# Kernel tuning notes

Hardware: AMD Instinct MI355X
Metric: run time of the kernel (lower is better)

The kernel has to match this reference:

```python
import jax, jax.numpy as jnp
import numpy as np

N_NODES = 100000
N_EDGES = 1600000


def gcn_conv(x, edge_index, W, b):
    """PyG-style GCNConv: self-loops + symmetric normalization + scatter-add."""
    n = x.shape[0]
    src, dst = edge_index[0], edge_index[1]
    loop = jnp.arange(n, dtype=src.dtype)
    src = jnp.concatenate([src, loop])
    dst = jnp.concatenate([dst, loop])
    h = x @ W  # [n, out] transform before propagate (PyG order)
    deg = jax.ops.segment_sum(jnp.ones_like(dst, dtype=h.dtype), dst, num_segments=n)
    dinv = jnp.where(deg > 0, deg ** -0.5, 0.0)
    norm = dinv[src] * dinv[dst]  # [E+n]
    msgs = h[src] * norm[:, None]  # gather + scale (largest intermediate)
    out = jax.ops.segment_sum(msgs, dst, num_segments=n)
    return out + b


def setup_inputs() -> dict:
    key = jax.random.key(0)
    ks = jax.random.split(key, 8)
    edge_attr = jax.random.normal(ks[0], (N_NODES, 5), dtype=jnp.float32)
    edge_index = jax.random.randint(ks[1], (2, N_EDGES), 0, N_NODES, dtype=jnp.int64)
    def lin(k, fan_in, fan_out):
        bound = 1.0 / np.sqrt(fan_in)
        return jax.random.uniform(k, (fan_in, fan_out), jnp.float32, -bound, bound)
    return {
        "edge_attr": edge_attr,
        "edge_index": edge_index,
        "W1": lin(ks[2], 5, 64),
        "b1": jnp.zeros((64,), jnp.float32),
        "W2": lin(ks[3], 64, 32),
        "b2": jnp.zeros((32,), jnp.float32),
        "fcW1": lin(ks[4], 32, 16),
        "fcb1": jnp.zeros((16,), jnp.float32),
        "fcW2": lin(ks[5], 16, 2),
        "fcb2": jnp.zeros((2,), jnp.float32),
    }


def reference(edge_attr, edge_index, W1, b1, W2, b2, fcW1, fcb1, fcW2, fcb2):
    x = jax.nn.relu(gcn_conv(edge_attr, edge_index, W1, b1))
    x = jax.nn.relu(gcn_conv(x, edge_index, W2, b2))
    x = jax.nn.relu(x @ fcW1 + fcb1)
    return x @ fcW2 + fcb2
```

## Files before the change

### kernel.cpp

```cpp
#include <hip/hip_runtime.h>


#define MS_TILE 2048
#define MAXB 512
#define AGG_NODES 32
#define AGG_STAGE 1024

__global__ __launch_bounds__(256) void histA(const int* __restrict__ dst,
                                             int* __restrict__ histG, int E) {
    __shared__ int h[MAXB];
    int t = threadIdx.x;
    h[t] = 0;
    h[t + 256] = 0;
    __syncthreads();
    int base = blockIdx.x * MS_TILE;
    int cnt = min(MS_TILE, E - base);
    for (int k = t; k < cnt; k += 256) atomicAdd(&h[dst[base + k] >> 8], 1);
    __syncthreads();
    histG[blockIdx.x * MAXB + t] = h[t];
    histG[blockIdx.x * MAXB + 256 + t] = h[t + 256];
}

__global__ __launch_bounds__(256) void scanTiles(const int* __restrict__ histG,
                                                 int* __restrict__ offsG,
                                                 int* __restrict__ bucketTotal,
                                                 int nTiles) {
    __shared__ int scn[256];
    int b = blockIdx.x, t = threadIdx.x;
    int run = 0;
    for (int base = 0; base < nTiles; base += 256) {
        int idx = base + t;
        int v = (idx < nTiles) ? histG[idx * MAXB + b] : 0;
        scn[t] = v;
        __syncthreads();
        int incl = v;
        for (int d = 1; d < 256; d <<= 1) {
            int add = (t >= d) ? scn[t - d] : 0;
            __syncthreads();
            incl += add;
            scn[t] = incl;
            __syncthreads();
        }
        if (idx < nTiles) offsG[idx * MAXB + b] = incl - v + run;
        run += scn[255];
        __syncthreads();
    }
    if (t == 0) bucketTotal[b] = run;
}

__global__ __launch_bounds__(256) void multisplit2(
    const int* __restrict__ src, const int* __restrict__ dst,
    const int* __restrict__ histG, const int* __restrict__ offsG,
    const int* __restrict__ btot, int* __restrict__ gbaseOut,
    unsigned* __restrict__ binned, int E) {
    __shared__ unsigned stage[MS_TILE];
    __shared__ unsigned short sb[MS_TILE];
    __shared__ int hoff[MAXB + 1];
    __shared__ int hcur[MAXB];
    __shared__ int gb[MAXB];
    __shared__ int scn[256];
    int t = threadIdx.x;
    int tile = blockIdx.x;
    int base = tile * MS_TILE;
    int cnt = min(MS_TILE, E - base);

    int b0 = btot[2 * t], b1v = btot[2 * t + 1];
    int s2 = b0 + b1v;
    scn[t] = s2;
    __syncthreads();
    int incl2 = s2;
    for (int d = 1; d < 256; d <<= 1) {
        int add = (t >= d) ? scn[t - d] : 0;
        __syncthreads();
        incl2 += add;
        scn[t] = incl2;
        __syncthreads();
    }
    int ex2 = incl2 - s2;
    gb[2 * t] = ex2 + offsG[tile * MAXB + 2 * t];
    gb[2 * t + 1] = ex2 + b0 + offsG[tile * MAXB + 2 * t + 1];
    if (tile == 0) {
        gbaseOut[2 * t] = ex2;
        gbaseOut[2 * t + 1] = ex2 + b0;
        if (t == 255) gbaseOut[MAXB] = E;
    }

    int a0 = histG[tile * MAXB + 2 * t];
    int a1 = histG[tile * MAXB + 2 * t + 1];
    int s = a0 + a1;
    scn[t] = s;
    __syncthreads();
    int incl = s;
    for (int d = 1; d < 256; d <<= 1) {
        int add = (t >= d) ? scn[t - d] : 0;
        __syncthreads();
        incl += add;
        scn[t] = incl;
        __syncthreads();
    }
    int ex = incl - s;
    hoff[2 * t] = ex;
    hoff[2 * t + 1] = ex + a0;
    hcur[2 * t] = ex;
    hcur[2 * t + 1] = ex + a0;
    if (t == 255) hoff[MAXB] = cnt;
    __syncthreads();
    for (int k = t; k < cnt; k += 256) {
        int d = dst[base + k];
        int b = d >> 8;
        int p = atomicAdd(&hcur[b], 1);
        stage[p] = ((unsigned)src[base + k] << 8) | (unsigned)(d & 255);
        sb[p] = (unsigned short)b;
    }
    __syncthreads();
    for (int k = t; k < cnt; k += 256) {
        int b = sb[k];
        binned[gb[b] + (k - hoff[b])] = stage[k];
    }
}

__global__ __launch_bounds__(256) void place_fine2(
    const unsigned* __restrict__ binned, const int* __restrict__ gbase,
    const float* __restrict__ x, int* __restrict__ offs,
    float* __restrict__ dinv, float* __restrict__ y, int* __restrict__ srcs, int n) {
    __shared__ int cnt[256];
    __shared__ int scn[256];
    __shared__ int lcur[256];
    int t = threadIdx.x, b = blockIdx.x;
    int node0 = b << 8;
    int nn = min(256, n - node0);
    int e0 = gbase[b], e1 = gbase[b + 1];
    cnt[t] = 0;
    __syncthreads();
    for (int k = e0 + t; k < e1; k += 256) atomicAdd(&cnt[binned[k] & 255u], 1);
    __syncthreads();
    int c = cnt[t];
    scn[t] = c;
    __syncthreads();
    int incl = c;
    for (int d = 1; d < 256; d <<= 1) {
        int add = (t >= d) ? scn[t - d] : 0;
        __syncthreads();
        incl += add;
        scn[t] = incl;
        __syncthreads();
    }
    int myoff = e0 + (incl - c);
    lcur[t] = myoff;
    if (t < nn) {
        int node = node0 + t;
        offs[node] = myoff;
        float di = 1.0f / sqrtf((float)(c + 1));
        dinv[node] = di;
        const float* xr = x + (size_t)node * 5;
        float4 a = {xr[0] * di, xr[1] * di, xr[2] * di, xr[3] * di};
        float4 bq = {xr[4] * di, 0.f, 0.f, 0.f};
        *(float4*)(y + (size_t)node * 8) = a;
        *(float4*)(y + (size_t)node * 8 + 4) = bq;
    }
    __syncthreads();
    for (int k = e0 + t; k < e1; k += 256) {
        unsigned w = binned[k];
        int p = atomicAdd(&lcur[w & 255u], 1);
        srcs[p] = (int)(w >> 8);
    }
}

__global__ __launch_bounds__(128) void agg_xin(
    const float* __restrict__ y, const int* __restrict__ srcs,
    const int* __restrict__ offs, const float* __restrict__ dinv,
    float* __restrict__ z, int n, int E) {
    int i = blockIdx.x * 128 + threadIdx.x;
    if (i >= n) return;
    const float4* yv = (const float4*)y;
    float4 a = yv[(size_t)i * 2];
    float4 b = yv[(size_t)i * 2 + 1];
    int off = offs[i];
    int cnt = ((i + 1 < n) ? offs[i + 1] : E) - off;
    int p = 0;
    for (; p + 4 <= cnt; p += 4) {
        int s0 = srcs[off + p], s1 = srcs[off + p + 1];
        int s2 = srcs[off + p + 2], s3 = srcs[off + p + 3];
        float4 v0 = yv[(size_t)s0 * 2];
        float4 w0 = yv[(size_t)s0 * 2 + 1];
        float4 v1 = yv[(size_t)s1 * 2];
        float4 w1 = yv[(size_t)s1 * 2 + 1];
        float4 v2 = yv[(size_t)s2 * 2];
        float4 w2 = yv[(size_t)s2 * 2 + 1];
        float4 v3 = yv[(size_t)s3 * 2];
        float4 w3 = yv[(size_t)s3 * 2 + 1];
        a.x += (v0.x + v1.x) + (v2.x + v3.x);
        a.y += (v0.y + v1.y) + (v2.y + v3.y);
        a.z += (v0.z + v1.z) + (v2.z + v3.z);
        a.w += (v0.w + v1.w) + (v2.w + v3.w);
        b.x += (w0.x + w1.x) + (w2.x + w3.x);
    }
    for (; p < cnt; ++p) {
        int s0 = srcs[off + p];
        float4 v0 = yv[(size_t)s0 * 2];
        float w0 = y[(size_t)s0 * 8 + 4];
        a.x += v0.x; a.y += v0.y; a.z += v0.z; a.w += v0.w;
        b.x += w0;
    }
    float di = dinv[i];
    float4 oa = {a.x * di, a.y * di, a.z * di, a.w * di};
    float4 ob = {b.x * di, 0.f, 0.f, 0.f};
    float4* zv = (float4*)z;
    zv[(size_t)i * 2] = oa;
    zv[(size_t)i * 2 + 1] = ob;
}

__global__ __launch_bounds__(256) void transform12(
    const float* __restrict__ z, const float* __restrict__ W1,
    const float* __restrict__ b1, const float* __restrict__ W2,
    const float* __restrict__ dinv, float* __restrict__ h2, int n) {
    __shared__ float w1s[320];
    __shared__ float b1s[64];
    __shared__ float w2s[64 * 32];
    __shared__ float o1[32 * 64];
    int t = threadIdx.x;
    w1s[t] = W1[t];
    if (t < 64) {
        w1s[t + 256] = W1[t + 256];
        b1s[t] = b1[t];
    }
#pragma unroll
    for (int r = 0; r < 8; ++r) w2s[r * 256 + t] = W2[r * 256 + t];
    __syncthreads();
    int node0 = blockIdx.x * 32;
#pragma unroll
    for (int r = 0; r < 8; ++r) {
        int idx = r * 256 + t;
        int li = idx >> 6, f = idx & 63;
        int i = node0 + li;
        if (i < n) {
            const float* zr = z + (size_t)i * 8;
            float acc = b1s[f];
#pragma unroll
            for (int k = 0; k < 5; ++k) acc += zr[k] * w1s[k * 64 + f];
            o1[li * 64 + f] = fmaxf(acc, 0.0f);
        }
    }
    __syncthreads();
#pragma unroll
    for (int r = 0; r < 4; ++r) {
        int idx = r * 256 + t;
        int li = idx >> 5, g = idx & 31;
        int i = node0 + li;
        if (i < n) {
            float acc = 0.f;
#pragma unroll
            for (int k = 0; k < 64; ++k) acc += o1[li * 64 + k] * w2s[k * 32 + g];
            h2[(size_t)i * 32 + g] = acc * dinv[i];
        }
    }
}

__global__ __launch_bounds__(256) void agg2_fc(
    const float* __restrict__ h, const int* __restrict__ srcs,
    const int* __restrict__ offs, const float* __restrict__ dinv,
    const float* __restrict__ b2, const float* __restrict__ fcW1,
    const float* __restrict__ fcb1, const float* __restrict__ fcW2,
    const float* __restrict__ fcb2, float* __restrict__ out, int n, int E) {
    __shared__ int sidx[AGG_STAGE];
    __shared__ float sm[AGG_NODES * 33];
    __shared__ float x3s[AGG_NODES * 16];
    __shared__ float w1s[512];
    __shared__ float w2s[32];
    __shared__ float b1s[16];
    __shared__ float b2s[2];
    __shared__ float bs2[32];
    int t = threadIdx.x;
    w1s[t] = fcW1[t];
    w1s[t + 256] = fcW1[t + 256];
    if (t < 32) { w2s[t] = fcW2[t]; bs2[t] = b2[t]; }
    if (t < 16) b1s[t] = fcb1[t];
    if (t < 2) b2s[t] = fcb2[t];

    int node0 = blockIdx.x * AGG_NODES;
    int li = t >> 3, fq = t & 7;
    int i = node0 + li;
    bool live = (i < n);
    const char* hb = (const char*)h;

    int e0 = offs[node0];
    int eEnd = (node0 + AGG_NODES < n) ? offs[node0 + AGG_NODES] : E;
    int myOff = 0, myCnt = 0;
    float4 acc = {0.f, 0.f, 0.f, 0.f};
    if (live) {
        myOff = offs[i];
        myCnt = ((i + 1 < n) ? offs[i + 1] : E) - myOff;
        acc = *(const float4*)(hb + ((size_t)i << 7) + (fq << 4));
    }

    for (int cs = e0; cs < eEnd; cs += AGG_STAGE) {
        int ce = min(cs + AGG_STAGE, eEnd);
        for (int k = cs + t; k < ce; k += 256) sidx[k - cs] = srcs[k] << 7;
        __syncthreads();
        int ps = max(myOff, cs), pe = min(myOff + myCnt, ce);
        int p = ps;
        for (; p + 8 <= pe; p += 8) {
            int o[8];
#pragma unroll
            for (int u = 0; u < 8; ++u) o[u] = sidx[p + u - cs];
            float4 v[8];
#pragma unroll
            for (int u = 0; u < 8; ++u)
                v[u] = *(const float4*)(hb + o[u] + (fq << 4));
#pragma unroll
            for (int u = 0; u < 8; ++u) {
                acc.x += v[u].x; acc.y += v[u].y;
                acc.z += v[u].z; acc.w += v[u].w;
            }
        }
        for (; p + 4 <= pe; p += 4) {
            int o0 = sidx[p - cs], o1 = sidx[p + 1 - cs];
            int o2 = sidx[p + 2 - cs], o3 = sidx[p + 3 - cs];
            float4 v0 = *(const float4*)(hb + o0 + (fq << 4));
            float4 v1 = *(const float4*)(hb + o1 + (fq << 4));
            float4 v2 = *(const float4*)(hb + o2 + (fq << 4));
            float4 v3 = *(const float4*)(hb + o3 + (fq << 4));
            acc.x += (v0.x + v1.x) + (v2.x + v3.x);
            acc.y += (v0.y + v1.y) + (v2.y + v3.y);
            acc.z += (v0.z + v1.z) + (v2.z + v3.z);
            acc.w += (v0.w + v1.w) + (v2.w + v3.w);
        }
        for (; p < pe; ++p) {
            float4 v = *(const float4*)(hb + sidx[p - cs] + (fq << 4));
            acc.x += v.x; acc.y += v.y; acc.z += v.z; acc.w += v.w;
        }
        __syncthreads();
    }

    if (live) {
        float di = dinv[i];
        int f0 = fq << 2;
        sm[li * 33 + f0 + 0] = fmaxf(di * acc.x + bs2[f0 + 0], 0.f);
        sm[li * 33 + f0 + 1] = fmaxf(di * acc.y + bs2[f0 + 1], 0.f);
        sm[li * 33 + f0 + 2] = fmaxf(di * acc.z + bs2[f0 + 2], 0.f);
        sm[li * 33 + f0 + 3] = fmaxf(di * acc.w + bs2[f0 + 3], 0.f);
    }
    __syncthreads();
#pragma unroll
    for (int r = 0; r < 2; ++r) {
        int idx = r * 256 + t;
        int lj = idx >> 4, j = idx & 15;
        if (node0 + lj < n) {
            float a = b1s[j];
#pragma unroll
            for (int k = 0; k < 32; ++k) a += sm[lj * 33 + k] * w1s[k * 16 + j];
            x3s[lj * 16 + j] = fmaxf(a, 0.f);
        }
    }
    __syncthreads();
    if (t < 64) {
        int lj = t >> 1, o = t & 1;
        if (node0 + lj < n) {
            float a = b2s[o];
#pragma unroll
            for (int j = 0; j < 16; ++j) a += x3s[lj * 16 + j] * w2s[j * 2 + o];
            out[(size_t)(node0 + lj) * 2 + o] = a;
        }
    }
}

extern "C" void kernel_launch(void* const* d_in, const int* in_sizes, int n_in,
                              void* d_out, int out_size, void* d_ws, size_t ws_size,
                              hipStream_t stream) {
    const float* edge_attr = (const float*)d_in[0];
    const int* edge_index  = (const int*)d_in[1];
    const float* W1   = (const float*)d_in[2];
    const float* b1   = (const float*)d_in[3];
    const float* W2   = (const float*)d_in[4];
    const float* b2   = (const float*)d_in[5];
    const float* fcW1 = (const float*)d_in[6];
    const float* fcb1 = (const float*)d_in[7];
    const float* fcW2 = (const float*)d_in[8];
    const float* fcb2 = (const float*)d_in[9];
    float* out = (float*)d_out;

    int n = in_sizes[0] / 5;
    int E = in_sizes[1] / 2;
    int NBkt = (n + 255) >> 8;
    int nTiles = (E + MS_TILE - 1) / MS_TILE;
    const int* src = edge_index;
    const int* dst = edge_index + E;

    char* ws = (char*)d_ws;
    auto alloc = [&](size_t bytes) {
        char* p = ws;
        ws += (bytes + 255) & ~(size_t)255;
        return p;
    };
    int*      offs   = (int*)alloc((size_t)n * 4);
    float*    dinv   = (float*)alloc((size_t)n * 4);
    int*      histG  = (int*)alloc((size_t)nTiles * MAXB * 4);
    int*      offsG  = (int*)alloc((size_t)nTiles * MAXB * 4);
    int*      btot   = (int*)alloc((size_t)MAXB * 4);
    int*      gbase  = (int*)alloc((size_t)(MAXB + 1) * 4);
    int*      srcs   = (int*)alloc((size_t)E * 4);
    unsigned* binned = (unsigned*)alloc((size_t)E * 4);
    float*    y      = (float*)alloc((size_t)n * 8 * 4);
    float*    z      = (float*)alloc((size_t)n * 8 * 4);
    float*    h2     = (float*)alloc((size_t)n * 32 * 4);

    histA<<<nTiles, 256, 0, stream>>>(dst, histG, E);
    scanTiles<<<MAXB, 256, 0, stream>>>(histG, offsG, btot, nTiles);
    multisplit2<<<nTiles, 256, 0, stream>>>(src, dst, histG, offsG, btot, gbase,
                                            binned, E);
    place_fine2<<<NBkt, 256, 0, stream>>>(binned, gbase, edge_attr, offs, dinv,
                                          y, srcs, n);
    agg_xin<<<(n + 127) / 128, 128, 0, stream>>>(y, srcs, offs, dinv, z, n, E);
    transform12<<<(n + 31) / 32, 256, 0, stream>>>(z, W1, b1, W2, dinv, h2, n);
    agg2_fc<<<(n + AGG_NODES - 1) / AGG_NODES, 256, 0, stream>>>(
        h2, srcs, offs, dinv, b2, fcW1, fcb1, fcW2, fcb2, out, n, E);
}
```

Baseline: 198.3 us.

## Split each node's edges across two thread groups in layer-2 aggregation; widen first gather

The fused layer-2 aggregation kernel now handles 16 nodes per block, giving each node 16 threads. Two 8-thread groups take alternate edges and combine their partial sums with a wave shuffle, which adds parallelism and memory-level parallelism for each node's gather. The layer-1 gather loop is unrolled from 4 to 8 edges and now loads only the five needed floats per neighbour instead of two full float4s. The risk is twice as many blocks, plus extra offset loads and the staging of srcs indices repeated across more blocks.

Measured after the change: 201.3 us. About the same (+1.5%).

```diff
diff --git a/kernel.cpp b/kernel.cpp
--- a/kernel.cpp
+++ b/kernel.cpp
@@ -3,7 +3,7 @@
 
 #define MS_TILE 2048
 #define MAXB 512
-#define AGG_NODES 32
+#define AGG_NODES 16
 #define AGG_STAGE 1024
 
 __global__ __launch_bounds__(256) void histA(const int* __restrict__ dst,
@@ -178,22 +178,22 @@
     int off = offs[i];
     int cnt = ((i + 1 < n) ? offs[i + 1] : E) - off;
     int p = 0;
-    for (; p + 4 <= cnt; p += 4) {
-        int s0 = srcs[off + p], s1 = srcs[off + p + 1];
-        int s2 = srcs[off + p + 2], s3 = srcs[off + p + 3];
-        float4 v0 = yv[(size_t)s0 * 2];
-        float4 w0 = yv[(size_t)s0 * 2 + 1];
-        float4 v1 = yv[(size_t)s1 * 2];
-        float4 w1 = yv[(size_t)s1 * 2 + 1];
-        float4 v2 = yv[(size_t)s2 * 2];
-        float4 w2 = yv[(size_t)s2 * 2 + 1];
-        float4 v3 = yv[(size_t)s3 * 2];
-        float4 w3 = yv[(size_t)s3 * 2 + 1];
-        a.x += (v0.x + v1.x) + (v2.x + v3.x);
-        a.y += (v0.y + v1.y) + (v2.y + v3.y);
-        a.z += (v0.z + v1.z) + (v2.z + v3.z);
-        a.w += (v0.w + v1.w) + (v2.w + v3.w);
-        b.x += (w0.x + w1.x) + (w2.x + w3.x);
+    for (; p + 8 <= cnt; p += 8) {
+        int s[8];
+#pragma unroll
+        for (int u = 0; u < 8; ++u) s[u] = srcs[off + p + u];
+        float4 v[8];
+        float w[8];
+#pragma unroll
+        for (int u = 0; u < 8; ++u) {
+            v[u] = yv[(size_t)s[u] * 2];
+            w[u] = y[(size_t)s[u] * 8 + 4];
+        }
+#pragma unroll
+        for (int u = 0; u < 8; ++u) {
+            a.x += v[u].x; a.y += v[u].y; a.z += v[u].z; a.w += v[u].w;
+            b.x += w[u];
+        }
     }
     for (; p < cnt; ++p) {
         int s0 = srcs[off + p];
@@ -278,7 +278,9 @@
     if (t < 2) b2s[t] = fcb2[t];
 
     int node0 = blockIdx.x * AGG_NODES;
-    int li = t >> 3, fq = t & 7;
+    int li = t >> 4;
+    int sub = (t >> 3) & 1;
+    int fq = t & 7;
     int i = node0 + li;
     bool live = (i < n);
     const char* hb = (const char*)h;
@@ -290,7 +292,8 @@
     if (live) {
         myOff = offs[i];
         myCnt = ((i + 1 < n) ? offs[i + 1] : E) - myOff;
-        acc = *(const float4*)(hb + ((size_t)i << 7) + (fq << 4));
+        if (sub == 0)
+            acc = *(const float4*)(hb + ((size_t)i << 7) + (fq << 4));
     }
 
     for (int cs = e0; cs < eEnd; cs += AGG_STAGE) {
@@ -298,24 +301,12 @@
         for (int k = cs + t; k < ce; k += 256) sidx[k - cs] = srcs[k] << 7;
         __syncthreads();
         int ps = max(myOff, cs), pe = min(myOff + myCnt, ce);
-        int p = ps;
-        for (; p + 8 <= pe; p += 8) {
-            int o[8];
-#pragma unroll
-            for (int u = 0; u < 8; ++u) o[u] = sidx[p + u - cs];
-            float4 v[8];
-#pragma unroll
-            for (int u = 0; u < 8; ++u)
-                v[u] = *(const float4*)(hb + o[u] + (fq << 4));
-#pragma unroll
-            for (int u = 0; u < 8; ++u) {
-                acc.x += v[u].x; acc.y += v[u].y;
-                acc.z += v[u].z; acc.w += v[u].w;
-            }
-        }
-        for (; p + 4 <= pe; p += 4) {
-            int o0 = sidx[p - cs], o1 = sidx[p + 1 - cs];
-            int o2 = sidx[p + 2 - cs], o3 = sidx[p + 3 - cs];
+        int p = ps + sub;
+        for (; p + 6 < pe; p += 8) {
+            int o0 = sidx[p - cs];
+            int o1 = sidx[p + 2 - cs];
+            int o2 = sidx[p + 4 - cs];
+            int o3 = sidx[p + 6 - cs];
             float4 v0 = *(const float4*)(hb + o0 + (fq << 4));
             float4 v1 = *(const float4*)(hb + o1 + (fq << 4));
             float4 v2 = *(const float4*)(hb + o2 + (fq << 4));
@@ -325,14 +316,19 @@
             acc.z += (v0.z + v1.z) + (v2.z + v3.z);
             acc.w += (v0.w + v1.w) + (v2.w + v3.w);
         }
-        for (; p < pe; ++p) {
+        for (; p < pe; p += 2) {
             float4 v = *(const float4*)(hb + sidx[p - cs] + (fq << 4));
             acc.x += v.x; acc.y += v.y; acc.z += v.z; acc.w += v.w;
         }
         __syncthreads();
     }
 
-    if (live) {
+    int lane = t & 63;
+    acc.x += __shfl(acc.x, lane ^ 8, 64);
+    acc.y += __shfl(acc.y, lane ^ 8, 64);
+    acc.z += __shfl(acc.z, lane ^ 8, 64);
+    acc.w += __shfl(acc.w, lane ^ 8, 64);
+    if (live && sub == 0) {
         float di = dinv[i];
         int f0 = fq << 2;
         sm[li * 33 + f0 + 0] = fmaxf(di * acc.x + bs2[f0 + 0], 0.f);
@@ -341,10 +337,8 @@
         sm[li * 33 + f0 + 3] = fmaxf(di * acc.w + bs2[f0 + 3], 0.f);
     }
     __syncthreads();
-#pragma unroll
-    for (int r = 0; r < 2; ++r) {
-        int idx = r * 256 + t;
-        int lj = idx >> 4, j = idx & 15;
+    {
+        int lj = t >> 4, j = t & 15;
         if (node0 + lj < n) {
             float a = b1s[j];
 #pragma unroll
@@ -353,7 +347,7 @@
         }
     }
     __syncthreads();
-    if (t < 64) {
+    if (t < 32) {
         int lj = t >> 1, o = t & 1;
         if (node0 + lj < n) {
             float a = b2s[o];
```

## Fuse all GCN stages into one cooperative persistent kernel with grid syncs

Applied to the files above, without the earlier changes.

Replaces the seven separate kernel launches with a single cooperative kernel that runs every stage as a grid-stride loop, with grid.sync() between stages. The aim is to remove per-launch overhead and the gaps between kernels. In exchange, the grid is capped at 768 persistent blocks, each block's shared memory is sized for the largest stage, and register pressure from the merged code may lower occupancy and parallelism in the bandwidth-bound gather stages.

Measured after the change: 604.2 us. +204.7%, slower.

```diff
diff --git a/kernel.cpp b/kernel.cpp
--- a/kernel.cpp
+++ b/kernel.cpp
@@ -1,365 +1,383 @@
 #include <hip/hip_runtime.h>
+#include <hip/hip_cooperative_groups.h>
+
+namespace cg = cooperative_groups;
 
 
 #define MS_TILE 2048
 #define MAXB 512
-#define AGG_NODES 32
 #define AGG_STAGE 1024
-
-__global__ __launch_bounds__(256) void histA(const int* __restrict__ dst,
-                                             int* __restrict__ histG, int E) {
-    __shared__ int h[MAXB];
+#define SMEM_BYTES 19712
+
+struct GcnParams {
+    const float* x;
+    const int* src;
+    const int* dst;
+    const float* W1; const float* b1;
+    const float* W2; const float* b2;
+    const float* fcW1; const float* fcb1;
+    const float* fcW2; const float* fcb2;
+    float* out;
+    int* histG; int* offsG; int* btot; int* gbase;
+    unsigned* binned; int* offs; float* dinv;
+    float* y; float* z; float* h2; int* srcs;
+    int n, E, nTiles, NBkt;
+};
+
+__global__ __launch_bounds__(256) void gcn_mono(GcnParams p) {
+    cg::grid_group grid = cg::this_grid();
+    __shared__ __align__(16) unsigned char smem[SMEM_BYTES];
     int t = threadIdx.x;
-    h[t] = 0;
-    h[t + 256] = 0;
-    __syncthreads();
-    int base = blockIdx.x * MS_TILE;
-    int cnt = min(MS_TILE, E - base);
-    for (int k = t; k < cnt; k += 256) atomicAdd(&h[dst[base + k] >> 8], 1);
-    __syncthreads();
-    histG[blockIdx.x * MAXB + t] = h[t];
-    histG[blockIdx.x * MAXB + 256 + t] = h[t + 256];
-}
-
-__global__ __launch_bounds__(256) void scanTiles(const int* __restrict__ histG,
-                                                 int* __restrict__ offsG,
-                                                 int* __restrict__ bucketTotal,
-                                                 int nTiles) {
-    __shared__ int scn[256];
-    int b = blockIdx.x, t = threadIdx.x;
-    int run = 0;
-    for (int base = 0; base < nTiles; base += 256) {
-        int idx = base + t;
-        int v = (idx < nTiles) ? histG[idx * MAXB + b] : 0;
-        scn[t] = v;
+    int G = gridDim.x;
+
+    {
+        int* h = (int*)smem;
+        for (int tile = blockIdx.x; tile < p.nTiles; tile += G) {
+            h[t] = 0;
+            h[t + 256] = 0;
+            __syncthreads();
+            int base = tile * MS_TILE;
+            int cnt = min(MS_TILE, p.E - base);
+            for (int k = t; k < cnt; k += 256) atomicAdd(&h[p.dst[base + k] >> 8], 1);
+            __syncthreads();
+            p.histG[tile * MAXB + t] = h[t];
+            p.histG[tile * MAXB + 256 + t] = h[t + 256];
+        }
+    }
+    grid.sync();
+
+    {
+        int* scn = (int*)smem;
+        for (int b = blockIdx.x; b < MAXB; b += G) {
+            int run = 0;
+            for (int base = 0; base < p.nTiles; base += 256) {
+                int idx = base + t;
+                int v = (idx < p.nTiles) ? p.histG[idx * MAXB + b] : 0;
+                scn[t] = v;
+                __syncthreads();
+                int incl = v;
+                for (int d = 1; d < 256; d <<= 1) {
+                    int add = (t >= d) ? scn[t - d] : 0;
+                    __syncthreads();
+                    incl += add;
+                    scn[t] = incl;
+                    __syncthreads();
+                }
+                if (idx < p.nTiles) p.offsG[idx * MAXB + b] = incl - v + run;
+                run += scn[255];
+                __syncthreads();
+            }
+            if (t == 0) p.btot[b] = run;
+        }
+    }
+    grid.sync();
+
+    {
+        unsigned* stage = (unsigned*)smem;
+        unsigned short* sb = (unsigned short*)(smem + 8192);
+        int* hoff = (int*)(smem + 12288);
+        int* hcur = (int*)(smem + 14344);
+        int* gb   = (int*)(smem + 16392);
+        int* scn  = (int*)(smem + 18440);
+        int b0 = p.btot[2 * t], b1v = p.btot[2 * t + 1];
+        int s2 = b0 + b1v;
+        scn[t] = s2;
         __syncthreads();
-        int incl = v;
+        int incl2 = s2;
         for (int d = 1; d < 256; d <<= 1) {
             int add = (t >= d) ? scn[t - d] : 0;
             __syncthreads();
-            incl += add;
-            scn[t] = incl;
-            __syncthreads();
-        }
-        if (idx < nTiles) offsG[idx * MAXB + b] = incl - v + run;
-        run += scn[255];
+            incl2 += add;
+            scn[t] = incl2;
+            __syncthreads();
+        }
+        int ex2a = incl2 - s2;
+        int ex2b = ex2a + b0;
+        if (blockIdx.x == 0) {
+            p.gbase[2 * t] = ex2a;
+            p.gbase[2 * t + 1] = ex2b;
+            if (t == 255) p.gbase[MAXB] = p.E;
+        }
+        for (int tile = blockIdx.x; tile < p.nTiles; tile += G) {
+            int base = tile * MS_TILE;
+            int cnt = min(MS_TILE, p.E - base);
+            int a0 = p.histG[tile * MAXB + 2 * t];
+            int a1 = p.histG[tile * MAXB + 2 * t + 1];
+            int s = a0 + a1;
+            scn[t] = s;
+            __syncthreads();
+            int incl = s;
+            for (int d = 1; d < 256; d <<= 1) {
+                int add = (t >= d) ? scn[t - d] : 0;
+                __syncthreads();
+                incl += add;
+                scn[t] = incl;
+                __syncthreads();
+            }
+            int ex = incl - s;
+            hoff[2 * t] = ex;
+            hoff[2 * t + 1] = ex + a0;
+            hcur[2 * t] = ex;
+            hcur[2 * t + 1] = ex + a0;
+            gb[2 * t] = ex2a + p.offsG[tile * MAXB + 2 * t];
+            gb[2 * t + 1] = ex2b + p.offsG[tile * MAXB + 2 * t + 1];
+            if (t == 255) hoff[MAXB] = cnt;
+            __syncthreads();
+            for (int k = t; k < cnt; k += 256) {
+                int d = p.dst[base + k];
+                int b = d >> 8;
+                int q = atomicAdd(&hcur[b], 1);
+                stage[q] = ((unsigned)p.src[base + k] << 8) | (unsigned)(d & 255);
+                sb[q] = (unsigned short)b;
+            }
+            __syncthreads();
+            for (int k = t; k < cnt; k += 256) {
+                int b = sb[k];
+                p.binned[gb[b] + (k - hoff[b])] = stage[k];
+            }
+        }
+    }
+    grid.sync();
+
+    {
+        int* cnt  = (int*)smem;
+        int* scn  = (int*)(smem + 1024);
+        int* lcur = (int*)(smem + 2048);
+        for (int b = blockIdx.x; b < p.NBkt; b += G) {
+            int node0 = b << 8;
+            int nn = min(256, p.n - node0);
+            int e0 = p.gbase[b], e1 = p.gbase[b + 1];
+            cnt[t] = 0;
+            __syncthreads();
+            for (int k = e0 + t; k < e1; k += 256)
+                atomicAdd(&cnt[p.binned[k] & 255u], 1);
+            __syncthreads();
+            int c = cnt[t];
+            scn[t] = c;
+            __syncthreads();
+            int incl = c;
+            for (int d = 1; d < 256; d <<= 1) {
+                int add = (t >= d) ? scn[t - d] : 0;
+                __syncthreads();
+                incl += add;
+                scn[t] = incl;
+                __syncthreads();
+            }
+            int myoff = e0 + (incl - c);
+            lcur[t] = myoff;
+            if (t < nn) {
+                int node = node0 + t;
+                p.offs[node] = myoff;
+                float di = 1.0f / sqrtf((float)(c + 1));
+                p.dinv[node] = di;
+                const float* xr = p.x + (size_t)node * 5;
+                float4 va = {xr[0] * di, xr[1] * di, xr[2] * di, xr[3] * di};
+                float4 vb = {xr[4] * di, 0.f, 0.f, 0.f};
+                *(float4*)(p.y + (size_t)node * 8) = va;
+                *(float4*)(p.y + (size_t)node * 8 + 4) = vb;
+            }
+            __syncthreads();
+            for (int k = e0 + t; k < e1; k += 256) {
+                unsigned w = p.binned[k];
+                int q = atomicAdd(&lcur[w & 255u], 1);
+                p.srcs[q] = (int)(w >> 8);
+            }
+            __syncthreads();
+        }
+    }
+    grid.sync();
+
+    {
+        const float4* yv = (const float4*)p.y;
+        for (int i = blockIdx.x * 256 + t; i < p.n; i += G * 256) {
+            float4 a = yv[(size_t)i * 2];
+            float4 b = yv[(size_t)i * 2 + 1];
+            int off = p.offs[i];
+            int cnt = ((i + 1 < p.n) ? p.offs[i + 1] : p.E) - off;
+            int q = 0;
+            for (; q + 4 <= cnt; q += 4) {
+                int s0 = p.srcs[off + q], s1 = p.srcs[off + q + 1];
+                int s2 = p.srcs[off + q + 2], s3 = p.srcs[off + q + 3];
+                float4 v0 = yv[(size_t)s0 * 2];
+                float4 w0 = yv[(size_t)s0 * 2 + 1];
+                float4 v1 = yv[(size_t)s1 * 2];
+                float4 w1 = yv[(size_t)s1 * 2 + 1];
+                float4 v2 = yv[(size_t)s2 * 2];
+                float4 w2 = yv[(size_t)s2 * 2 + 1];
+                float4 v3 = yv[(size_t)s3 * 2];
+                float4 w3 = yv[(size_t)s3 * 2 + 1];
+                a.x += (v0.x + v1.x) + (v2.x + v3.x);
+                a.y += (v0.y + v1.y) + (v2.y + v3.y);
+                a.z += (v0.z + v1.z) + (v2.z + v3.z);
+                a.w += (v0.w + v1.w) + (v2.w + v3.w);
+                b.x += (w0.x + w1.x) + (w2.x + w3.x);
+            }
+            for (; q < cnt; ++q) {
+                int s0 = p.srcs[off + q];
+                float4 v0 = yv[(size_t)s0 * 2];
+                float w0 = p.y[(size_t)s0 * 8 + 4];
+                a.x += v0.x; a.y += v0.y; a.z += v0.z; a.w += v0.w;
+                b.x += w0;
+            }
+            float di = p.dinv[i];
+            float4 oa = {a.x * di, a.y * di, a.z * di, a.w * di};
+            float4 ob = {b.x * di, 0.f, 0.f, 0.f};
+            ((float4*)p.z)[(size_t)i * 2] = oa;
+            ((float4*)p.z)[(size_t)i * 2 + 1] = ob;
+        }
+    }
+    grid.sync();
+
+    {
+        float* w1s = (float*)smem;
+        float* b1s = (float*)(smem + 1280);
+        float* w2s = (float*)(smem + 1536);
+        float* o1  = (float*)(smem + 9728);
+        w1s[t] = p.W1[t];
+        if (t < 64) {
+            w1s[t + 256] = p.W1[t + 256];
+            b1s[t] = p.b1[t];
+        }
+#pragma unroll
+        for (int r = 0; r < 8; ++r) w2s[r * 256 + t] = p.W2[r * 256 + t];
         __syncthreads();
-    }
-    if (t == 0) bucketTotal[b] = run;
-}
-
-__global__ __launch_bounds__(256) void multisplit2(
-    const int* __restrict__ src, const int* __restrict__ dst,
-    const int* __restrict__ histG, const int* __restrict__ offsG,
-    const int* __restrict__ btot, int* __restrict__ gbaseOut,
-    unsigned* __restrict__ binned, int E) {
-    __shared__ unsigned stage[MS_TILE];
-    __shared__ unsigned short sb[MS_TILE];
-    __shared__ int hoff[MAXB + 1];
-    __shared__ int hcur[MAXB];
-    __shared__ int gb[MAXB];
-    __shared__ int scn[256];
-    int t = threadIdx.x;
-    int tile = blockIdx.x;
-    int base = tile * MS_TILE;
-    int cnt = min(MS_TILE, E - base);
-
-    int b0 = btot[2 * t], b1v = btot[2 * t + 1];
-    int s2 = b0 + b1v;
-    scn[t] = s2;
-    __syncthreads();
-    int incl2 = s2;
-    for (int d = 1; d < 256; d <<= 1) {
-        int add = (t >= d) ? scn[t - d] : 0;
+        int nChunks = (p.n + 31) / 32;
+        for (int c = blockIdx.x; c < nChunks; c += G) {
+            int node0 = c * 32;
+#pragma unroll
+            for (int r = 0; r < 8; ++r) {
+                int idx = r * 256 + t;
+                int li = idx >> 6, f = idx & 63;
+                int i = node0 + li;
+                if (i < p.n) {
+                    const float* zr = p.z + (size_t)i * 8;
+                    float acc = b1s[f];
+#pragma unroll
+                    for (int k = 0; k < 5; ++k) acc += zr[k] * w1s[k * 64 + f];
+                    o1[li * 64 + f] = fmaxf(acc, 0.0f);
+                }
+            }
+            __syncthreads();
+#pragma unroll
+            for (int r = 0; r < 4; ++r) {
+                int idx = r * 256 + t;
+                int li = idx >> 5, g = idx & 31;
+                int i = node0 + li;
+                if (i < p.n) {
+                    float acc = 0.f;
+#pragma unroll
+                    for (int k = 0; k < 64; ++k)
+                        acc += o1[li * 64 + k] * w2s[k * 32 + g];
+                    p.h2[(size_t)i * 32 + g] = acc * p.dinv[i];
+                }
+            }
+            __syncthreads();
+        }
+    }
+    grid.sync();
+
+    {
+        int* sidx  = (int*)smem;
+        float* sm  = (float*)(smem + 4096);
+        float* x3s = (float*)(smem + 8320);
+        float* w1s = (float*)(smem + 10368);
+        float* w2s = (float*)(smem + 12416);
+        float* b1s = (float*)(smem + 12544);
+        float* b2s = (float*)(smem + 12608);
+        float* bs2 = (float*)(smem + 12624);
+        w1s[t] = p.fcW1[t];
+        w1s[t + 256] = p.fcW1[t + 256];
+        if (t < 32) { w2s[t] = p.fcW2[t]; bs2[t] = p.b2[t]; }
+        if (t < 16) b1s[t] = p.fcb1[t];
+        if (t < 2) b2s[t] = p.fcb2[t];
         __syncthreads();
-        incl2 += add;
-        scn[t] = incl2;
-        __syncthreads();
-    }
-    int ex2 = incl2 - s2;
-    gb[2 * t] = ex2 + offsG[tile * MAXB + 2 * t];
-    gb[2 * t + 1] = ex2 + b0 + offsG[tile * MAXB + 2 * t + 1];
-    if (tile == 0) {
-        gbaseOut[2 * t] = ex2;
-        gbaseOut[2 * t + 1] = ex2 + b0;
-        if (t == 255) gbaseOut[MAXB] = E;
-    }
-
-    int a0 = histG[tile * MAXB + 2 * t];
-    int a1 = histG[tile * MAXB + 2 * t + 1];
-    int s = a0 + a1;
-    scn[t] = s;
-    __syncthreads();
-    int incl = s;
-    for (int d = 1; d < 256; d <<= 1) {
-        int add = (t >= d) ? scn[t - d] : 0;
-        __syncthreads();
-        incl += add;
-        scn[t] = incl;
-        __syncthreads();
-    }
-    int ex = incl - s;
-    hoff[2 * t] = ex;
-    hoff[2 * t + 1] = ex + a0;
-    hcur[2 * t] = ex;
-    hcur[2 * t + 1] = ex + a0;
-    if (t == 255) hoff[MAXB] = cnt;
-    __syncthreads();
-    for (int k = t; k < cnt; k += 256) {
-        int d = dst[base + k];
-        int b = d >> 8;
-        int p = atomicAdd(&hcur[b], 1);
-        stage[p] = ((unsigned)src[base + k] << 8) | (unsigned)(d & 255);
-        sb[p] = (unsigned short)b;
-    }
-    __syncthreads();
-    for (int k = t; k < cnt; k += 256) {
-        int b = sb[k];
-        binned[gb[b] + (k - hoff[b])] = stage[k];
-    }
-}
-
-__global__ __launch_bounds__(256) void place_fine2(
-    const unsigned* __restrict__ binned, const int* __restrict__ gbase,
-    const float* __restrict__ x, int* __restrict__ offs,
-    float* __restrict__ dinv, float* __restrict__ y, int* __restrict__ srcs, int n) {
-    __shared__ int cnt[256];
-    __shared__ int scn[256];
-    __shared__ int lcur[256];
-    int t = threadIdx.x, b = blockIdx.x;
-    int node0 = b << 8;
-    int nn = min(256, n - node0);
-    int e0 = gbase[b], e1 = gbase[b + 1];
-    cnt[t] = 0;
-    __syncthreads();
-    for (int k = e0 + t; k < e1; k += 256) atomicAdd(&cnt[binned[k] & 255u], 1);
-    __syncthreads();
-    int c = cnt[t];
-    scn[t] = c;
-    __syncthreads();
-    int incl = c;
-    for (int d = 1; d < 256; d <<= 1) {
-        int add = (t >= d) ? scn[t - d] : 0;
-        __syncthreads();
-        incl += add;
-        scn[t] = incl;
-        __syncthreads();
-    }
-    int myoff = e0 + (incl - c);
-    lcur[t] = myoff;
-    if (t < nn) {
-        int node = node0 + t;
-        offs[node] = myoff;
-        float di = 1.0f / sqrtf((float)(c + 1));
-        dinv[node] = di;
-        const float* xr = x + (size_t)node * 5;
-        float4 a = {xr[0] * di, xr[1] * di, xr[2] * di, xr[3] * di};
-        float4 bq = {xr[4] * di, 0.f, 0.f, 0.f};
-        *(float4*)(y + (size_t)node * 8) = a;
-        *(float4*)(y + (size_t)node * 8 + 4) = bq;
-    }
-    __syncthreads();
-    for (int k = e0 + t; k < e1; k += 256) {
-        unsigned w = binned[k];
-        int p = atomicAdd(&lcur[w & 255u], 1);
-        srcs[p] = (int)(w >> 8);
-    }
-}
-
-__global__ __launch_bounds__(128) void agg_xin(
-    const float* __restrict__ y, const int* __restrict__ srcs,
-    const int* __restrict__ offs, const float* __restrict__ dinv,
-    float* __restrict__ z, int n, int E) {
-    int i = blockIdx.x * 128 + threadIdx.x;
-    if (i >= n) return;
-    const float4* yv = (const float4*)y;
-    float4 a = yv[(size_t)i * 2];
-    float4 b = yv[(size_t)i * 2 + 1];
-    int off = offs[i];
-    int cnt = ((i + 1 < n) ? offs[i + 1] : E) - off;
-    int p = 0;
-    for (; p + 4 <= cnt; p += 4) {
-        int s0 = srcs[off + p], s1 = srcs[off + p + 1];
-        int s2 = srcs[off + p + 2], s3 = srcs[off + p + 3];
-        float4 v0 = yv[(size_t)s0 * 2];
-        float4 w0 = yv[(size_t)s0 * 2 + 1];
-        float4 v1 = yv[(size_t)s1 * 2];
-        float4 w1 = yv[(size_t)s1 * 2 + 1];
-        float4 v2 = yv[(size_t)s2 * 2];
-        float4 w2 = yv[(size_t)s2 * 2 + 1];
-        float4 v3 = yv[(size_t)s3 * 2];
-        float4 w3 = yv[(size_t)s3 * 2 + 1];
-        a.x += (v0.x + v1.x) + (v2.x + v3.x);
-        a.y += (v0.y + v1.y) + (v2.y + v3.y);
-        a.z += (v0.z + v1.z) + (v2.z + v3.z);
-        a.w += (v0.w + v1.w) + (v2.w + v3.w);
-        b.x += (w0.x + w1.x) + (w2.x + w3.x);
-    }
-    for (; p < cnt; ++p) {
-        int s0 = srcs[off + p];
-        float4 v0 = yv[(size_t)s0 * 2];
-        float w0 = y[(size_t)s0 * 8 + 4];
-        a.x += v0.x; a.y += v0.y; a.z += v0.z; a.w += v0.w;
-        b.x += w0;
-    }
-    float di = dinv[i];
-    float4 oa = {a.x * di, a.y * di, a.z * di, a.w * di};
-    float4 ob = {b.x * di, 0.f, 0.f, 0.f};
-    float4* zv = (float4*)z;
-    zv[(size_t)i * 2] = oa;
-    zv[(size_t)i * 2 + 1] = ob;
-}
-
-__global__ __launch_bounds__(256) void transform12(
-    const float* __restrict__ z, const float* __restrict__ W1,
-    const float* __restrict__ b1, const float* __restrict__ W2,
-    const float* __restrict__ dinv, float* __restrict__ h2, int n) {
-    __shared__ float w1s[320];
-    __shared__ float b1s[64];
-    __shared__ float w2s[64 * 32];
-    __shared__ float o1[32 * 64];
-    int t = threadIdx.x;
-    w1s[t] = W1[t];
-    if (t < 64) {
-        w1s[t + 256] = W1[t + 256];
-        b1s[t] = b1[t];
-    }
-#pragma unroll
-    for (int r = 0; r < 8; ++r) w2s[r * 256 + t] = W2[r * 256 + t];
-    __syncthreads();
-    int node0 = blockIdx.x * 32;
-#pragma unroll
-    for (int r = 0; r < 8; ++r) {
-        int idx = r * 256 + t;
-        int li = idx >> 6, f = idx & 63;
-        int i = node0 + li;
-        if (i < n) {
-            const float* zr = z + (size_t)i * 8;
-            float acc = b1s[f];
-#pragma unroll
-            for (int k = 0; k < 5; ++k) acc += zr[k] * w1s[k * 64 + f];
-            o1[li * 64 + f] = fmaxf(acc, 0.0f);
-        }
-    }
-    __syncthreads();
-#pragma unroll
-    for (int r = 0; r < 4; ++r) {
-        int idx = r * 256 + t;
-        int li = idx >> 5, g = idx & 31;
-        int i = node0 + li;
-        if (i < n) {
-            float acc = 0.f;
-#pragma unroll
-            for (int k = 0; k < 64; ++k) acc += o1[li * 64 + k] * w2s[k * 32 + g];
-            h2[(size_t)i * 32 + g] = acc * dinv[i];
-        }
-    }
-}
-
-__global__ __launch_bounds__(256) void agg2_fc(
-    const float* __restrict__ h, const int* __restrict__ srcs,
-    const int* __restrict__ offs, const float* __restrict__ dinv,
-    const float* __restrict__ b2, const float* __restrict__ fcW1,
-    const float* __restrict__ fcb1, const float* __restrict__ fcW2,
-    const float* __restrict__ fcb2, float* __restrict__ out, int n, int E) {
-    __shared__ int sidx[AGG_STAGE];
-    __shared__ float sm[AGG_NODES * 33];
-    __shared__ float x3s[AGG_NODES * 16];
-    __shared__ float w1s[512];
-    __shared__ float w2s[32];
-    __shared__ float b1s[16];
-    __shared__ float b2s[2];
-    __shared__ float bs2[32];
-    int t = threadIdx.x;
-    w1s[t] = fcW1[t];
-    w1s[t + 256] = fcW1[t + 256];
-    if (t < 32) { w2s[t] = fcW2[t]; bs2[t] = b2[t]; }
-    if (t < 16) b1s[t] = fcb1[t];
-    if (t < 2) b2s[t] = fcb2[t];
-
-    int node0 = blockIdx.x * AGG_NODES;
-    int li = t >> 3, fq = t & 7;
-    int i = node0 + li;
-    bool live = (i < n);
-    const char* hb = (const char*)h;
-
-    int e0 = offs[node0];
-    int eEnd = (node0 + AGG_NODES < n) ? offs[node0 + AGG_NODES] : E;
-    int myOff = 0, myCnt = 0;
-    float4 acc = {0.f, 0.f, 0.f, 0.f};
-    if (live) {
-        myOff = offs[i];
-        myCnt = ((i + 1 < n) ? offs[i + 1] : E) - myOff;
-        acc = *(const float4*)(hb + ((size_t)i << 7) + (fq << 4));
-    }
-
-    for (int cs = e0; cs < eEnd; cs += AGG_STAGE) {
-        int ce = min(cs + AGG_STAGE, eEnd);
-        for (int k = cs + t; k < ce; k += 256) sidx[k - cs] = srcs[k] << 7;
-        __syncthreads();
-        int ps = max(myOff, cs), pe = min(myOff + myCnt, ce);
-        int p = ps;
-        for (; p + 8 <= pe; p += 8) {
-            int o[8];
-#pragma unroll
-            for (int u = 0; u < 8; ++u) o[u] = sidx[p + u - cs];
-            float4 v[8];
-#pragma unroll
-            for (int u = 0; u < 8; ++u)
-                v[u] = *(const float4*)(hb + o[u] + (fq << 4));
-#pragma unroll
-            for (int u = 0; u < 8; ++u) {
-                acc.x += v[u].x; acc.y += v[u].y;
-                acc.z += v[u].z; acc.w += v[u].w;
-            }
-        }
-        for (; p + 4 <= pe; p += 4) {
-            int o0 = sidx[p - cs], o1 = sidx[p + 1 - cs];
-            int o2 = sidx[p + 2 - cs], o3 = sidx[p + 3 - cs];
-            float4 v0 = *(const float4*)(hb + o0 + (fq << 4));
-            float4 v1 = *(const float4*)(hb + o1 + (fq << 4));
-            float4 v2 = *(const float4*)(hb + o2 + (fq << 4));
-            float4 v3 = *(const float4*)(hb + o3 + (fq << 4));
-            acc.x += (v0.x + v1.x) + (v2.x + v3.x);
-            acc.y += (v0.y + v1.y) + (v2.y + v3.y);
-            acc.z += (v0.z + v1.z) + (v2.z + v3.z);
-            acc.w += (v0.w + v1.w) + (v2.w + v3.w);
-        }
-        for (; p < pe; ++p) {
-            float4 v = *(const float4*)(hb + sidx[p - cs] + (fq << 4));
-            acc.x += v.x; acc.y += v.y; acc.z += v.z; acc.w += v.w;
-        }
-        __syncthreads();
-    }
-
-    if (live) {
-        float di = dinv[i];
-        int f0 = fq << 2;
-        sm[li * 33 + f0 + 0] = fmaxf(di * acc.x + bs2[f0 + 0], 0.f);
-        sm[li * 33 + f0 + 1] = fmaxf(di * acc.y + bs2[f0 + 1], 0.f);
-        sm[li * 33 + f0 + 2] = fmaxf(di * acc.z + bs2[f0 + 2], 0.f);
-        sm[li * 33 + f0 + 3] = fmaxf(di * acc.w + bs2[f0 + 3], 0.f);
-    }
-    __syncthreads();
-#pragma unroll
-    for (int r = 0; r < 2; ++r) {
-        int idx = r * 256 + t;
-        int lj = idx >> 4, j = idx & 15;
-        if (node0 + lj < n) {
-            float a = b1s[j];
-#pragma unroll
-            for (int k = 0; k < 32; ++k) a += sm[lj * 33 + k] * w1s[k * 16 + j];
-            x3s[lj * 16 + j] = fmaxf(a, 0.f);
-        }
-    }
-    __syncthreads();
-    if (t < 64) {
-        int lj = t >> 1, o = t & 1;
-        if (node0 + lj < n) {
-            float a = b2s[o];
-#pragma unroll
-            for (int j = 0; j < 16; ++j) a += x3s[lj * 16 + j] * w2s[j * 2 + o];
-            out[(size_t)(node0 + lj) * 2 + o] = a;
+        const char* hb = (const char*)p.h2;
+        int li = t >> 3, fq = t & 7;
+        int nBlk = (p.n + 31) / 32;
+        for (int bb = blockIdx.x; bb < nBlk; bb += G) {
+            int node0 = bb * 32;
+            int i = node0 + li;
+            bool live = (i < p.n);
+            int e0 = p.offs[node0];
+            int eEnd = (node0 + 32 < p.n) ? p.offs[node0 + 32] : p.E;
+            int myOff = 0, myCnt = 0;
+            float4 acc = {0.f, 0.f, 0.f, 0.f};
+            if (live) {
+                myOff = p.offs[i];
+                myCnt = ((i + 1 < p.n) ? p.offs[i + 1] : p.E) - myOff;
+                acc = *(const float4*)(hb + ((size_t)i << 7) + (fq << 4));
+            }
+            for (int cs = e0; cs < eEnd; cs += AGG_STAGE) {
+                int ce = min(cs + AGG_STAGE, eEnd);
+                for (int k = cs + t; k < ce; k += 256) sidx[k - cs] = p.srcs[k] << 7;
+                __syncthreads();
+                int ps = max(myOff, cs), pe = min(myOff + myCnt, ce);
+                int q = ps;
+                for (; q + 8 <= pe; q += 8) {
+                    int o[8];
+#pragma unroll
+                    for (int u = 0; u < 8; ++u) o[u] = sidx[q + u - cs];
+                    float4 v[8];
+#pragma unroll
+                    for (int u = 0; u < 8; ++u)
+                        v[u] = *(const float4*)(hb + o[u] + (fq << 4));
+#pragma unroll
+                    for (int u = 0; u < 8; ++u) {
+                        acc.x += v[u].x; acc.y += v[u].y;
+                        acc.z += v[u].z; acc.w += v[u].w;
+                    }
+                }
+                for (; q + 4 <= pe; q += 4) {
+                    int o0 = sidx[q - cs], o1 = sidx[q + 1 - cs];
+                    int o2 = sidx[q + 2 - cs], o3 = sidx[q + 3 - cs];
+                    float4 v0 = *(const float4*)(hb + o0 + (fq << 4));
+                    float4 v1 = *(const float4*)(hb + o1 + (fq << 4));
+                    float4 v2 = *(const float4*)(hb + o2 + (fq << 4));
+                    float4 v3 = *(const float4*)(hb + o3 + (fq << 4));
+                    acc.x += (v0.x + v1.x) + (v2.x + v3.x);
+                    acc.y += (v0.y + v1.y) + (v2.y + v3.y);
+                    acc.z += (v0.z + v1.z) + (v2.z + v3.z);
+                    acc.w += (v0.w + v1.w) + (v2.w + v3.w);
+                }
+                for (; q < pe; ++q) {
+                    float4 v = *(const float4*)(hb + sidx[q - cs] + (fq << 4));
+                    acc.x += v.x; acc.y += v.y; acc.z += v.z; acc.w += v.w;
+                }
+                __syncthreads();
+            }
+            if (live) {
+                float di = p.dinv[i];
+                int f0 = fq << 2;
+                sm[li * 33 + f0 + 0] = fmaxf(di * acc.x + bs2[f0 + 0], 0.f);
+                sm[li * 33 + f0 + 1] = fmaxf(di * acc.y + bs2[f0 + 1], 0.f);
+                sm[li * 33 + f0 + 2] = fmaxf(di * acc.z + bs2[f0 + 2], 0.f);
+                sm[li * 33 + f0 + 3] = fmaxf(di * acc.w + bs2[f0 + 3], 0.f);
+            }
+            __syncthreads();
+#pragma unroll
+            for (int r = 0; r < 2; ++r) {
+                int idx = r * 256 + t;
+                int lj = idx >> 4, j = idx & 15;
+                if (node0 + lj < p.n) {
+                    float a = b1s[j];
+#pragma unroll
+                    for (int k = 0; k < 32; ++k)
+                        a += sm[lj * 33 + k] * w1s[k * 16 + j];
+                    x3s[lj * 16 + j] = fmaxf(a, 0.f);
+                }
+            }
+            __syncthreads();
+            if (t < 64) {
+                int lj = t >> 1, o = t & 1;
+                if (node0 + lj < p.n) {
+                    float a = b2s[o];
+#pragma unroll
+                    for (int j = 0; j < 16; ++j)
+                        a += x3s[lj * 16 + j] * w2s[j * 2 + o];
+                    p.out[(size_t)(node0 + lj) * 2 + o] = a;
+                }
+            }
+            __syncthreads();
         }
     }
 }
@@ -367,51 +385,52 @@
 extern "C" void kernel_launch(void* const* d_in, const int* in_sizes, int n_in,
                               void* d_out, int out_size, void* d_ws, size_t ws_size,
                               hipStream_t stream) {
-    const float* edge_attr = (const float*)d_in[0];
-    const int* edge_index  = (const int*)d_in[1];
-    const float* W1   = (const float*)d_in[2];
-    const float* b1   = (const float*)d_in[3];
-    const float* W2   = (const float*)d_in[4];
-    const float* b2   = (const float*)d_in[5];
-    const float* fcW1 = (const float*)d_in[6];
-    const float* fcb1 = (const float*)d_in[7];
-    const float* fcW2 = (const float*)d_in[8];
-    const float* fcb2 = (const float*)d_in[9];
-    float* out = (float*)d_out;
-
-    int n = in_sizes[0] / 5;
-    int E = in_sizes[1] / 2;
-    int NBkt = (n + 255) >> 8;
-    int nTiles = (E + MS_TILE - 1) / MS_TILE;
-    const int* src = edge_index;
-    const int* dst = edge_index + E;
+    GcnParams p;
+    p.x    = (const float*)d_in[0];
+    const int* edge_index = (const int*)d_in[1];
+    p.W1   = (const float*)d_in[2];
+    p.b1   = (const float*)d_in[3];
+    p.W2   = (const float*)d_in[4];
+    p.b2   = (const float*)d_in[5];
+    p.fcW1 = (const float*)d_in[6];
+    p.fcb1 = (const float*)d_in[7];
+    p.fcW2 = (const float*)d_in[8];
+    p.fcb2 = (const float*)d_in[9];
+    p.out  = (float*)d_out;
+
+    p.n = in_sizes[0] / 5;
+    p.E = in_sizes[1] / 2;
+    p.NBkt = (p.n + 255) >> 8;
+    p.nTiles = (p.E + MS_TILE - 1) / MS_TILE;
+    p.src = edge_index;
+    p.dst = edge_index + p.E;
 
     char* ws = (char*)d_ws;
     auto alloc = [&](size_t bytes) {
-        char* p = ws;
+        char* q = ws;
         ws += (bytes + 255) & ~(size_t)255;
-        return p;
+        return q;
     };
-    int*      offs   = (int*)alloc((size_t)n * 4);
-    float*    dinv   = (float*)alloc((size_t)n * 4);
-    int*      histG  = (int*)alloc((size_t)nTiles * MAXB * 4);
-    int*      offsG  = (int*)alloc((size_t)nTiles * MAXB * 4);
-    int*      btot   = (int*)alloc((size_t)MAXB * 4);
-    int*      gbase  = (int*)alloc((size_t)(MAXB + 1) * 4);
-    int*      srcs   = (int*)alloc((size_t)E * 4);
-    unsigned* binned = (unsigned*)alloc((size_t)E * 4);
-    float*    y      = (float*)alloc((size_t)n * 8 * 4);
-    float*    z      = (float*)alloc((size_t)n * 8 * 4);
-    float*    h2     = (float*)alloc((size_t)n * 32 * 4);
-
-    histA<<<nTiles, 256, 0, stream>>>(dst, histG, E);
-    scanTiles<<<MAXB, 256, 0, stream>>>(histG, offsG, btot, nTiles);
-    multisplit2<<<nTiles, 256, 0, stream>>>(src, dst, histG, offsG, btot, gbase,
-                                            binned, E);
-    place_fine2<<<NBkt, 256, 0, stream>>>(binned, gbase, edge_attr, offs, dinv,
-                                          y, srcs, n);
-    agg_xin<<<(n + 127) / 128, 128, 0, stream>>>(y, srcs, offs, dinv, z, n, E);
-    transform12<<<(n + 31) / 32, 256, 0, stream>>>(z, W1, b1, W2, dinv, h2, n);
-    agg2_fc<<<(n + AGG_NODES - 1) / AGG_NODES, 256, 0, stream>>>(
-        h2, srcs, offs, dinv, b2, fcW1, fcb1, fcW2, fcb2, out, n, E);
+    p.offs   = (int*)alloc((size_t)p.n * 4);
+    p.dinv   = (float*)alloc((size_t)p.n * 4);
+    p.histG  = (int*)alloc((size_t)p.nTiles * MAXB * 4);
+    p.offsG  = (int*)alloc((size_t)p.nTiles * MAXB * 4);
+    p.btot   = (int*)alloc((size_t)MAXB * 4);
+    p.gbase  = (int*)alloc((size_t)(MAXB + 1) * 4);
+    p.srcs   = (int*)alloc((size_t)p.E * 4);
+    p.binned = (unsigned*)alloc((size_t)p.E * 4);
+    p.y      = (float*)alloc((size_t)p.n * 8 * 4);
+    p.z      = (float*)alloc((size_t)p.n * 8 * 4);
+    p.h2     = (float*)alloc((size_t)p.n * 32 * 4);
+
+    int maxPerCU = 0;
+    hipOccupancyMaxActiveBlocksPerMultiprocessor(&maxPerCU, (const void*)gcn_mono,
+                                                 256, 0);
+    if (maxPerCU < 1) maxPerCU = 1;
+    int grid = maxPerCU * 256;
+    if (grid > 768) grid = 768;
+
+    void* args[] = {&p};
+    hipLaunchCooperativeKernel((void*)gcn_mono, dim3(grid), dim3(256), args, 0,
+                               stream);
 }
```

## Fuse first-layer aggregation into transform kernel with 8 lanes per node

Applied to the files above, without the earlier changes.

Merges the layer-1 neighbor aggregation kernel into the dense transform kernel. Each node's edges are now split across 8 lanes and combined with warp shuffles, and the aggregated result is kept in shared memory instead of being written to and read back from a global z buffer. This removes one kernel launch and the z round trip, and spreads the gather work across more threads. In exchange, the transform kernel becomes heavier, and lanes in a group sit idle when a node has few edges.

New measurement: 186.1 us. 1.07x faster.

```diff
diff --git a/kernel.cpp b/kernel.cpp
--- a/kernel.cpp
+++ b/kernel.cpp
@@ -166,58 +166,16 @@
     }
 }
 
-__global__ __launch_bounds__(128) void agg_xin(
+__global__ __launch_bounds__(256) void agg1_t12(
     const float* __restrict__ y, const int* __restrict__ srcs,
     const int* __restrict__ offs, const float* __restrict__ dinv,
-    float* __restrict__ z, int n, int E) {
-    int i = blockIdx.x * 128 + threadIdx.x;
-    if (i >= n) return;
-    const float4* yv = (const float4*)y;
-    float4 a = yv[(size_t)i * 2];
-    float4 b = yv[(size_t)i * 2 + 1];
-    int off = offs[i];
-    int cnt = ((i + 1 < n) ? offs[i + 1] : E) - off;
-    int p = 0;
-    for (; p + 4 <= cnt; p += 4) {
-        int s0 = srcs[off + p], s1 = srcs[off + p + 1];
-        int s2 = srcs[off + p + 2], s3 = srcs[off + p + 3];
-        float4 v0 = yv[(size_t)s0 * 2];
-        float4 w0 = yv[(size_t)s0 * 2 + 1];
-        float4 v1 = yv[(size_t)s1 * 2];
-        float4 w1 = yv[(size_t)s1 * 2 + 1];
-        float4 v2 = yv[(size_t)s2 * 2];
-        float4 w2 = yv[(size_t)s2 * 2 + 1];
-        float4 v3 = yv[(size_t)s3 * 2];
-        float4 w3 = yv[(size_t)s3 * 2 + 1];
-        a.x += (v0.x + v1.x) + (v2.x + v3.x);
-        a.y += (v0.y + v1.y) + (v2.y + v3.y);
-        a.z += (v0.z + v1.z) + (v2.z + v3.z);
-        a.w += (v0.w + v1.w) + (v2.w + v3.w);
-        b.x += (w0.x + w1.x) + (w2.x + w3.x);
-    }
-    for (; p < cnt; ++p) {
-        int s0 = srcs[off + p];
-        float4 v0 = yv[(size_t)s0 * 2];
-        float w0 = y[(size_t)s0 * 8 + 4];
-        a.x += v0.x; a.y += v0.y; a.z += v0.z; a.w += v0.w;
-        b.x += w0;
-    }
-    float di = dinv[i];
-    float4 oa = {a.x * di, a.y * di, a.z * di, a.w * di};
-    float4 ob = {b.x * di, 0.f, 0.f, 0.f};
-    float4* zv = (float4*)z;
-    zv[(size_t)i * 2] = oa;
-    zv[(size_t)i * 2 + 1] = ob;
-}
-
-__global__ __launch_bounds__(256) void transform12(
-    const float* __restrict__ z, const float* __restrict__ W1,
-    const float* __restrict__ b1, const float* __restrict__ W2,
-    const float* __restrict__ dinv, float* __restrict__ h2, int n) {
+    const float* __restrict__ W1, const float* __restrict__ b1,
+    const float* __restrict__ W2, float* __restrict__ h2, int n, int E) {
     __shared__ float w1s[320];
     __shared__ float b1s[64];
     __shared__ float w2s[64 * 32];
     __shared__ float o1[32 * 64];
+    __shared__ float zs[32 * 6];
     int t = threadIdx.x;
     w1s[t] = W1[t];
     if (t < 64) {
@@ -226,32 +184,69 @@
     }
 #pragma unroll
     for (int r = 0; r < 8; ++r) w2s[r * 256 + t] = W2[r * 256 + t];
-    __syncthreads();
+
     int node0 = blockIdx.x * 32;
+    int li = t >> 3, e = t & 7;
+    int i = node0 + li;
+    const float4* yv = (const float4*)y;
+    float4 a = {0.f, 0.f, 0.f, 0.f};
+    float b0 = 0.f;
+    if (i < n) {
+        int off = offs[i];
+        int cnt = ((i + 1 < n) ? offs[i + 1] : E) - off;
+        if (e == 0) {
+            a = yv[(size_t)i * 2];
+            b0 = y[(size_t)i * 8 + 4];
+        }
+        for (int p = e; p < cnt; p += 8) {
+            int s = srcs[off + p];
+            float4 v = yv[(size_t)s * 2];
+            float w = y[(size_t)s * 8 + 4];
+            a.x += v.x; a.y += v.y; a.z += v.z; a.w += v.w;
+            b0 += w;
+        }
+    }
+#pragma unroll
+    for (int m = 4; m >= 1; m >>= 1) {
+        a.x += __shfl_xor(a.x, m, 64);
+        a.y += __shfl_xor(a.y, m, 64);
+        a.z += __shfl_xor(a.z, m, 64);
+        a.w += __shfl_xor(a.w, m, 64);
+        b0  += __shfl_xor(b0, m, 64);
+    }
+    if (i < n && e == 0) {
+        float di = dinv[i];
+        zs[li * 6 + 0] = a.x * di;
+        zs[li * 6 + 1] = a.y * di;
+        zs[li * 6 + 2] = a.z * di;
+        zs[li * 6 + 3] = a.w * di;
+        zs[li * 6 + 4] = b0 * di;
+        zs[li * 6 + 5] = di;
+    }
+    __syncthreads();
 #pragma unroll
     for (int r = 0; r < 8; ++r) {
         int idx = r * 256 + t;
-        int li = idx >> 6, f = idx & 63;
-        int i = node0 + li;
-        if (i < n) {
-            const float* zr = z + (size_t)i * 8;
+        int lj = idx >> 6, f = idx & 63;
+        if (node0 + lj < n) {
+            const float* zr = zs + lj * 6;
             float acc = b1s[f];
 #pragma unroll
             for (int k = 0; k < 5; ++k) acc += zr[k] * w1s[k * 64 + f];
-            o1[li * 64 + f] = fmaxf(acc, 0.0f);
+            o1[lj * 64 + f] = fmaxf(acc, 0.0f);
         }
     }
     __syncthreads();
 #pragma unroll
     for (int r = 0; r < 4; ++r) {
         int idx = r * 256 + t;
-        int li = idx >> 5, g = idx & 31;
-        int i = node0 + li;
-        if (i < n) {
+        int lj = idx >> 5, g = idx & 31;
+        int i2 = node0 + lj;
+        if (i2 < n) {
             float acc = 0.f;
 #pragma unroll
-            for (int k = 0; k < 64; ++k) acc += o1[li * 64 + k] * w2s[k * 32 + g];
-            h2[(size_t)i * 32 + g] = acc * dinv[i];
+            for (int k = 0; k < 64; ++k) acc += o1[lj * 64 + k] * w2s[k * 32 + g];
+            h2[(size_t)i2 * 32 + g] = acc * zs[lj * 6 + 5];
         }
     }
 }
@@ -401,7 +396,6 @@
     int*      srcs   = (int*)alloc((size_t)E * 4);
     unsigned* binned = (unsigned*)alloc((size_t)E * 4);
     float*    y      = (float*)alloc((size_t)n * 8 * 4);
-    float*    z      = (float*)alloc((size_t)n * 8 * 4);
     float*    h2     = (float*)alloc((size_t)n * 32 * 4);
 
     histA<<<nTiles, 256, 0, stream>>>(dst, histG, E);
@@ -410,8 +404,8 @@
                                             binned, E);
     place_fine2<<<NBkt, 256, 0, stream>>>(binned, gbase, edge_attr, offs, dinv,
                                           y, srcs, n);
-    agg_xin<<<(n + 127) / 128, 128, 0, stream>>>(y, srcs, offs, dinv, z, n, E);
-    transform12<<<(n + 31) / 32, 256, 0, stream>>>(z, W1, b1, W2, dinv, h2, n);
+    agg1_t12<<<(n + 31) / 32, 256, 0, stream>>>(y, srcs, offs, dinv, W1, b1, W2,
+                                                h2, n, E);
     agg2_fc<<<(n + AGG_NODES - 1) / AGG_NODES, 256, 0, stream>>>(
         h2, srcs, offs, dinv, b2, fcW1, fcb1, fcW2, fcb2, out, n, E);
 }
```
